# Performance work log

Hardware: AMD Instinct MI355X
Metric: run time of the kernel (lower is better)

## Reference

```python
import jax, jax.numpy as jnp
import numpy as np

D_MODEL = 1024
NUM_HEADS = 16
HEAD_DIM = D_MODEL // NUM_HEADS
B, N = 4, 2048


def setup_inputs() -> dict:
    key = jax.random.key(0)
    ks = jax.random.split(key, 9)
    s = 1.0 / np.sqrt(D_MODEL)
    inp = {
        "x": jax.random.normal(ks[0], (B, N, D_MODEL), dtype=jnp.float32),
        "Wq": jax.random.normal(ks[1], (D_MODEL, D_MODEL), dtype=jnp.float32) * s,
        "bq": jnp.zeros((D_MODEL,), dtype=jnp.float32),
        "Wk": jax.random.normal(ks[2], (D_MODEL, D_MODEL), dtype=jnp.float32) * s,
        "bk": jnp.zeros((D_MODEL,), dtype=jnp.float32),
        "Wv": jax.random.normal(ks[3], (D_MODEL, D_MODEL), dtype=jnp.float32) * s,
        "bv": jnp.zeros((D_MODEL,), dtype=jnp.float32),
        "Wo": jax.random.normal(ks[4], (D_MODEL, D_MODEL), dtype=jnp.float32) * s,
        "bo": jnp.zeros((D_MODEL,), dtype=jnp.float32),
    }
    return inp


def reference(x, Wq, bq, Wk, bk, Wv, bv, Wo, bo):
    b, n, c = x.shape
    h, d = NUM_HEADS, HEAD_DIM
    # QKV projections -> [B, H, N, d]
    q = (x @ Wq + bq).reshape(b, n, h, d).transpose(0, 2, 1, 3)
    k = (x @ Wk + bk).reshape(b, n, h, d).transpose(0, 2, 1, 3)
    v = (x @ Wv + bv).reshape(b, n, h, d).transpose(0, 2, 1, 3)
    scores = jnp.einsum("bhqd,bhkd->bhqk", q, k) / np.sqrt(d).astype(jnp.float32)
    attn = jax.nn.softmax(scores, axis=-1)  # dropout p=0 -> identity
    out = jnp.einsum("bhqk,bhkd->bhqd", attn, v)
    out = out.transpose(0, 2, 1, 3).reshape(b, n, c)
    return out @ Wo + bo
```

## Files before the change

### kernel.cpp

```cpp
#include <hip/hip_runtime.h>
#include <hip/hip_bf16.h>
#include <stdint.h>

#define DM 1024
#define SEQL 2048
#define NBATCH 4
#define NHEAD 16
#define HDIM 64
#define MTOT (NBATCH * SEQL)

using f32x4 = __attribute__((ext_vector_type(4))) float;
using f32x16 = __attribute__((ext_vector_type(16))) float;
using bf16x8 = __attribute__((ext_vector_type(8))) short;

static __device__ __forceinline__ unsigned short f2bf(float f) {
  union { float f; uint32_t u; } v; v.f = f;
  uint32_t u = v.u;
  return (unsigned short)((u + 0x7FFFu + ((u >> 16) & 1u)) >> 16);
}

static __device__ __forceinline__ float exp2_fast(float x) {
#if __has_builtin(__builtin_amdgcn_exp2f)
  return __builtin_amdgcn_exp2f(x);
#else
  float r;
  asm("v_exp_f32 %0, %1" : "=v"(r) : "v"(x));
  return r;
#endif
}

static __device__ __forceinline__ uint32_t pkbf(float lo, float hi) {
  float2 f; f.x = lo; f.y = hi;
  __hip_bfloat162 h = __float22bfloat162_rn(f);
  union { __hip_bfloat162 h; uint32_t u; } cv; cv.h = h;
  return cv.u;
}

static __device__ __forceinline__ f32x16 zero16() {
  f32x16 z;
#pragma unroll
  for (int i = 0; i < 16; ++i) z[i] = 0.f;
  return z;
}

static __device__ __forceinline__ void gload16(const void* g, void* l) {
  __builtin_amdgcn_global_load_lds(
      (const __attribute__((address_space(1))) unsigned int*)g,
      (__attribute__((address_space(3))) unsigned int*)l,
      16, 0, 0);
}

__global__ __launch_bounds__(256) void transpose_convert4(
    const float* __restrict__ W0, const float* __restrict__ W1,
    const float* __restrict__ W2, const float* __restrict__ W3,
    unsigned short* __restrict__ T0, unsigned short* __restrict__ T1,
    unsigned short* __restrict__ T2, unsigned short* __restrict__ T3) {
  __shared__ float tile[64][65];
  const int z = blockIdx.z;
  const float* W = z == 0 ? W0 : z == 1 ? W1 : z == 2 ? W2 : W3;
  unsigned short* WT = z == 0 ? T0 : z == 1 ? T1 : z == 2 ? T2 : T3;
  const int bx = blockIdx.x;
  const int by = blockIdx.y;
  const int t = threadIdx.x;
  const int r = t >> 4;
  const int c4 = (t & 15) * 4;
#pragma unroll
  for (int i = 0; i < 4; ++i) {
    const float4 v = *reinterpret_cast<const float4*>(
        &W[(size_t)(by * 64 + r + i * 16) * DM + bx * 64 + c4]);
    tile[r + i * 16][c4 + 0] = v.x;
    tile[r + i * 16][c4 + 1] = v.y;
    tile[r + i * 16][c4 + 2] = v.z;
    tile[r + i * 16][c4 + 3] = v.w;
  }
  __syncthreads();
#pragma unroll
  for (int i = 0; i < 4; ++i) {
    const int rr = r + i * 16;
    uint32_t lo = (uint32_t)f2bf(tile[c4 + 0][rr]) | ((uint32_t)f2bf(tile[c4 + 1][rr]) << 16);
    uint32_t hi = (uint32_t)f2bf(tile[c4 + 2][rr]) | ((uint32_t)f2bf(tile[c4 + 3][rr]) << 16);
    uint2 o; o.x = lo; o.y = hi;
    *reinterpret_cast<uint2*>(&WT[(size_t)(bx * 64 + rr) * DM + by * 64 + c4]) = o;
  }
}

__global__ __launch_bounds__(256) void convert_x(
    const float* __restrict__ x, unsigned short* __restrict__ xb) {
  const int i = blockIdx.x * 256 + threadIdx.x;
  const float4 v = reinterpret_cast<const float4*>(x)[i];
  uint2 o;
  o.x = (uint32_t)f2bf(v.x) | ((uint32_t)f2bf(v.y) << 16);
  o.y = (uint32_t)f2bf(v.z) | ((uint32_t)f2bf(v.w) << 16);
  reinterpret_cast<uint2*>(xb)[i] = o;
}

#define QSCALE 0.1803368801111204f

__global__ __launch_bounds__(256) void gemm_qkv(
    const unsigned short* __restrict__ A, const unsigned short* __restrict__ BT,
    const float* __restrict__ bq, const float* __restrict__ bk, const float* __restrict__ bv,
    unsigned short* __restrict__ qo, unsigned short* __restrict__ ko,
    unsigned short* __restrict__ vo) {
  __shared__ unsigned short As[128][64];
  __shared__ unsigned short Bs[128][64];
  const int tid = threadIdx.x;
  const int w = tid >> 6;
  const int lane = tid & 63;
  const int wm = w >> 1, wn = w & 1;
  const int m0 = blockIdx.y * 128;
  const int n0 = blockIdx.x * 128;
  const int mode = n0 >> 10;
  const int lrow = lane & 15;
  const int lk = (lane >> 4) * 8;
  const int sRow = lane >> 3;
  const int sCol = (lane & 7) * 8;

  unsigned short* dstA = (mode == 2) ? &Bs[0][0] : &As[0][0];
  unsigned short* dstB = (mode == 2) ? &As[0][0] : &Bs[0][0];

  f32x4 acc[4][4];
#pragma unroll
  for (int m = 0; m < 4; ++m)
#pragma unroll
    for (int n = 0; n < 4; ++n) acc[m][n] = (f32x4){0.f, 0.f, 0.f, 0.f};

  for (int k0 = 0; k0 < DM; k0 += 64) {
#pragma unroll
    for (int i = 0; i < 4; ++i) {
      const int rb = i * 32 + w * 8;
      gload16(&A[(size_t)(m0 + rb + sRow) * DM + k0 + sCol], dstA + rb * 64);
    }
#pragma unroll
    for (int i = 0; i < 4; ++i) {
      const int rb = i * 32 + w * 8;
      gload16(&BT[(size_t)(n0 + rb + sRow) * DM + k0 + sCol], dstB + rb * 64);
    }
    __syncthreads();
#pragma unroll
    for (int ks = 0; ks < 2; ++ks) {
      bf16x8 af[4], bfr[4];
#pragma unroll
      for (int m = 0; m < 4; ++m)
        af[m] = *reinterpret_cast<const bf16x8*>(&As[wm * 64 + m * 16 + lrow][ks * 32 + lk]);
#pragma unroll
      for (int n = 0; n < 4; ++n)
        bfr[n] = *reinterpret_cast<const bf16x8*>(&Bs[wn * 64 + n * 16 + lrow][ks * 32 + lk]);
#pragma unroll
      for (int m = 0; m < 4; ++m)
#pragma unroll
        for (int n = 0; n < 4; ++n)
          acc[m][n] = __builtin_amdgcn_mfma_f32_16x16x32_bf16(af[m], bfr[n], acc[m][n], 0, 0, 0);
    }
    __syncthreads();
  }

  if (mode < 2) {
    const bool isK = (mode == 1);
    unsigned short* dst = isK ? ko : qo;
    const float* bp = isK ? bk : bq;
    const float sc = isK ? 1.f : QSCALE;
#pragma unroll
    for (int n = 0; n < 4; ++n) {
      const int col = (n0 & 1023) + wn * 64 + n * 16 + lrow;
      const float bb = bp[col];
      const int hh = col >> 6, dd = col & 63;
#pragma unroll
      for (int m = 0; m < 4; ++m) {
        const int rowb = m0 + wm * 64 + m * 16 + (lane >> 4) * 4;
#pragma unroll
        for (int r = 0; r < 4; ++r) {
          const int mg = rowb + r;
          const int bidx = mg >> 11;
          const int nn = mg & 2047;
          dst[((size_t)(bidx * NHEAD + hh) * SEQL + nn) * HDIM + dd] =
              f2bf((acc[m][n][r] + bb) * sc);
        }
      }
    }
  } else {
#pragma unroll
    for (int m = 0; m < 4; ++m) {
#pragma unroll
      for (int r = 0; r < 4; ++r) {
        const int dv = (n0 - 2048) + wm * 64 + m * 16 + (lane >> 4) * 4 + r;
        const float bb = bv[dv];
        const int hh = dv >> 6, dd = dv & 63;
#pragma unroll
        for (int n = 0; n < 4; ++n) {
          const int seq = m0 + wn * 64 + n * 16 + lrow;
          const int bidx = seq >> 11;
          const int nn = seq & 2047;
          vo[((size_t)(bidx * NHEAD + hh) * HDIM + dd) * SEQL + nn] =
              f2bf(acc[m][n][r] + bb);
        }
      }
    }
  }
}

__global__ __launch_bounds__(256) void gemm_out(
    const unsigned short* __restrict__ A, const unsigned short* __restrict__ BT,
    const float* __restrict__ bias, float* __restrict__ Cout) {
  __shared__ unsigned short As[128][64];
  __shared__ unsigned short Bs[128][64];
  const int tid = threadIdx.x;
  const int w = tid >> 6;
  const int lane = tid & 63;
  const int wm = w >> 1, wn = w & 1;
  const int m0 = (blockIdx.x >> 3) * 128;
  const int n0 = (blockIdx.x & 7) * 128;
  const int lrow = lane & 15;
  const int lk = (lane >> 4) * 8;
  const int sRow = lane >> 3;
  const int sCol = (lane & 7) * 8;

  f32x4 acc[4][4];
#pragma unroll
  for (int m = 0; m < 4; ++m)
#pragma unroll
    for (int n = 0; n < 4; ++n) acc[m][n] = (f32x4){0.f, 0.f, 0.f, 0.f};

  for (int k0 = 0; k0 < DM; k0 += 64) {
#pragma unroll
    for (int i = 0; i < 4; ++i) {
      const int rb = i * 32 + w * 8;
      gload16(&A[(size_t)(m0 + rb + sRow) * DM + k0 + sCol], &As[rb][0]);
    }
#pragma unroll
    for (int i = 0; i < 4; ++i) {
      const int rb = i * 32 + w * 8;
      gload16(&BT[(size_t)(n0 + rb + sRow) * DM + k0 + sCol], &Bs[rb][0]);
    }
    __syncthreads();
#pragma unroll
    for (int ks = 0; ks < 2; ++ks) {
      bf16x8 af[4], bfr[4];
#pragma unroll
      for (int m = 0; m < 4; ++m)
        af[m] = *reinterpret_cast<const bf16x8*>(&As[wm * 64 + m * 16 + lrow][ks * 32 + lk]);
#pragma unroll
      for (int n = 0; n < 4; ++n)
        bfr[n] = *reinterpret_cast<const bf16x8*>(&Bs[wn * 64 + n * 16 + lrow][ks * 32 + lk]);
#pragma unroll
      for (int m = 0; m < 4; ++m)
#pragma unroll
        for (int n = 0; n < 4; ++n)
          acc[m][n] = __builtin_amdgcn_mfma_f32_16x16x32_bf16(af[m], bfr[n], acc[m][n], 0, 0, 0);
    }
    __syncthreads();
  }

#pragma unroll
  for (int n = 0; n < 4; ++n) {
    const int col = n0 + wn * 64 + n * 16 + lrow;
    const float bb = bias[col];
#pragma unroll
    for (int m = 0; m < 4; ++m) {
      const int rowb = m0 + wm * 64 + m * 16 + (lane >> 4) * 4;
#pragma unroll
      for (int r = 0; r < 4; ++r) {
        Cout[(size_t)(rowb + r) * DM + col] = acc[m][n][r] + bb;
      }
    }
  }
}

__global__ __launch_bounds__(512) void attn_kernel(
    const unsigned short* __restrict__ q, const unsigned short* __restrict__ k,
    const unsigned short* __restrict__ vt, unsigned short* __restrict__ attn_out) {
  __shared__ unsigned short Ks[4][64 * 64];
  __shared__ unsigned short Vs[4][64 * 64];

  const int bid = blockIdx.x;
  const int l0 = (bid & 7) * 64 + (bid >> 3);
  const int bh = l0 >> 3;
  const int qt = l0 & 7;
  const int b = bh >> 4, h = bh & 15;

  const int tid = threadIdx.x;
  const int w = tid >> 6;
  const int lane = tid & 63;
  const int qv = lane & 31;
  const int hi = lane >> 5;
  const int qg0 = qt * 256 + w * 32;

  const unsigned short* qptr = q + (size_t)bh * SEQL * HDIM;
  const unsigned short* kptr = k + (size_t)bh * SEQL * HDIM;
  const unsigned short* vptr = vt + (size_t)bh * HDIM * SEQL;

  bf16x8 qb[4];
#pragma unroll
  for (int kc = 0; kc < 4; ++kc)
    qb[kc] = *reinterpret_cast<const bf16x8*>(&qptr[(qg0 + qv) * HDIM + kc * 16 + hi * 8]);

  bf16x8 ones;
#pragma unroll
  for (int i = 0; i < 8; ++i) ones[i] = (short)0x3F80;

  f32x16 acc0 = zero16(), acc1 = zero16(), accL = zero16();

  const int x7 = qv & 7;
  int off[4];
#pragma unroll
  for (int i = 0; i < 4; ++i) off[i] = ((2 * i + hi) ^ x7) << 3;

  const int srow = tid >> 3;
  const int sslot = tid & 7;
  const int sdst = srow * 64 + ((sslot ^ (srow & 7)) << 3);

  uint4 rk0, rk1, rv0, rv1;
#define LOADT2(rr)                                                                       \
  {                                                                                      \
    rk0 = *reinterpret_cast<const uint4*>(&kptr[((rr) * 128 + srow) * HDIM + sslot * 8]);     \
    rk1 = *reinterpret_cast<const uint4*>(&kptr[((rr) * 128 + 64 + srow) * HDIM + sslot * 8]);\
    rv0 = *reinterpret_cast<const uint4*>(&vptr[srow * SEQL + (rr) * 128 + sslot * 8]);       \
    rv1 = *reinterpret_cast<const uint4*>(&vptr[srow * SEQL + (rr) * 128 + 64 + sslot * 8]);  \
  }

  LOADT2(0);
  const int NR = SEQL / 128;
  for (int r = 0; r < NR; ++r) {
    const int s = (r & 1) << 1;
    *reinterpret_cast<uint4*>(&Ks[s][sdst]) = rk0;
    *reinterpret_cast<uint4*>(&Ks[s + 1][sdst]) = rk1;
    *reinterpret_cast<uint4*>(&Vs[s][sdst]) = rv0;
    *reinterpret_cast<uint4*>(&Vs[s + 1][sdst]) = rv1;
    __syncthreads();
    if (r + 1 < NR) LOADT2(r + 1);

#pragma unroll
    for (int half = 0; half < 2; ++half) {
      const int c = s + half;

      f32x16 p0 = zero16(), p1 = zero16();
      __builtin_amdgcn_s_setprio(1);
#pragma unroll
      for (int kc = 0; kc < 4; ++kc) {
        bf16x8 ka0 = *reinterpret_cast<const bf16x8*>(&Ks[c][qv * 64 + off[kc]]);
        bf16x8 ka1 = *reinterpret_cast<const bf16x8*>(&Ks[c][(32 + qv) * 64 + off[kc]]);
        p0 = __builtin_amdgcn_mfma_f32_32x32x16_bf16(ka0, qb[kc], p0, 0, 0, 0);
        p1 = __builtin_amdgcn_mfma_f32_32x32x16_bf16(ka1, qb[kc], p1, 0, 0, 0);
      }
      __builtin_amdgcn_s_setprio(0);

#pragma unroll
      for (int i = 0; i < 16; ++i) {
        p0[i] = exp2_fast(p0[i]);
        p1[i] = exp2_fast(p1[i]);
      }

      bf16x8 pa[4];
#pragma unroll
      for (int ks = 0; ks < 4; ++ks) {
        const int o = 8 * (ks & 1);
        uint32_t X1, X2, Y1, Y2;
        if (ks < 2) {
          X1 = pkbf(p0[o + 0], p0[o + 1]); X2 = pkbf(p0[o + 2], p0[o + 3]);
          Y1 = pkbf(p0[o + 4], p0[o + 5]); Y2 = pkbf(p0[o + 6], p0[o + 7]);
        } else {
          X1 = pkbf(p1[o + 0], p1[o + 1]); X2 = pkbf(p1[o + 2], p1[o + 3]);
          Y1 = pkbf(p1[o + 4], p1[o + 5]); Y2 = pkbf(p1[o + 6], p1[o + 7]);
        }
        asm("v_permlane32_swap_b32 %0, %1" : "+v"(X1), "+v"(Y1));
        asm("v_permlane32_swap_b32 %0, %1" : "+v"(X2), "+v"(Y2));
        union { uint32_t u[4]; bf16x8 v; } uu;
        uu.u[0] = X1; uu.u[1] = X2; uu.u[2] = Y1; uu.u[3] = Y2;
        pa[ks] = uu.v;
      }

      __builtin_amdgcn_s_setprio(1);
#pragma unroll
      for (int ks = 0; ks < 4; ++ks) {
        bf16x8 vb0 = *reinterpret_cast<const bf16x8*>(&Vs[c][qv * 64 + off[ks]]);
        bf16x8 vb1 = *reinterpret_cast<const bf16x8*>(&Vs[c][(32 + qv) * 64 + off[ks]]);
        acc0 = __builtin_amdgcn_mfma_f32_32x32x16_bf16(pa[ks], vb0, acc0, 0, 0, 0);
        acc1 = __builtin_amdgcn_mfma_f32_32x32x16_bf16(pa[ks], vb1, acc1, 0, 0, 0);
        accL = __builtin_amdgcn_mfma_f32_32x32x16_bf16(pa[ks], ones, accL, 0, 0, 0);
      }
      __builtin_amdgcn_s_setprio(0);
    }
  }
#undef LOADT2

#pragma unroll
  for (int rg = 0; rg < 16; ++rg) {
    const int crow = (rg & 3) + 8 * (rg >> 2) + 4 * hi;
    const float invl = 1.f / accL[rg];
    const int qg = qg0 + crow;
    const size_t base = ((size_t)(b * SEQL + qg) * NHEAD + h) * HDIM + qv;
    attn_out[base] = f2bf(acc0[rg] * invl);
    attn_out[base + 32] = f2bf(acc1[rg] * invl);
  }
}

extern "C" void kernel_launch(void* const* d_in, const int* in_sizes, int n_in,
                              void* d_out, int out_size, void* d_ws, size_t ws_size,
                              hipStream_t stream) {
  const float* x  = (const float*)d_in[0];
  const float* Wq = (const float*)d_in[1];
  const float* bq = (const float*)d_in[2];
  const float* Wk = (const float*)d_in[3];
  const float* bk = (const float*)d_in[4];
  const float* Wv = (const float*)d_in[5];
  const float* bv = (const float*)d_in[6];
  const float* Wo = (const float*)d_in[7];
  const float* bo = (const float*)d_in[8];

  char* ws = (char*)d_ws;
  unsigned short* wqT = (unsigned short*)(ws);
  unsigned short* wkT = wqT + 1024 * 1024;
  unsigned short* wvT = wkT + 1024 * 1024;
  unsigned short* woT = wvT + 1024 * 1024;
  unsigned short* xb   = (unsigned short*)(ws + (size_t)(8 << 20));
  unsigned short* attn = xb;
  unsigned short* qw   = (unsigned short*)(ws + (size_t)(24 << 20));
  unsigned short* kw   = (unsigned short*)(ws + (size_t)(40 << 20));
  unsigned short* vtw  = (unsigned short*)(ws + (size_t)(56 << 20));

  transpose_convert4<<<dim3(16, 16, 4), 256, 0, stream>>>(Wq, Wk, Wv, Wo, wqT, wkT, wvT, woT);
  convert_x<<<MTOT * DM / 4 / 256, 256, 0, stream>>>(x, xb);

  gemm_qkv<<<dim3(24, 64), 256, 0, stream>>>(xb, wqT, bq, bk, bv, qw, kw, vtw);

  attn_kernel<<<512, 512, 0, stream>>>(qw, kw, vtw, attn);

  gemm_out<<<512, 256, 0, stream>>>(attn, woT, bo, (float*)d_out);
}
```

Measured before the change: 202.9 us.

## Double-buffer A tile with XOR swizzle and read weight fragments directly from global

```diff
diff --git a/kernel.cpp b/kernel.cpp
--- a/kernel.cpp
+++ b/kernel.cpp
@@ -101,8 +101,7 @@
     const float* __restrict__ bq, const float* __restrict__ bk, const float* __restrict__ bv,
     unsigned short* __restrict__ qo, unsigned short* __restrict__ ko,
     unsigned short* __restrict__ vo) {
-  __shared__ unsigned short As[128][64];
-  __shared__ unsigned short Bs[128][64];
+  __shared__ unsigned short As[2][128 * 64];
   const int tid = threadIdx.x;
   const int w = tid >> 6;
   const int lane = tid & 63;
@@ -111,12 +110,18 @@
   const int n0 = blockIdx.x * 128;
   const int mode = n0 >> 10;
   const int lrow = lane & 15;
-  const int lk = (lane >> 4) * 8;
+  const int lhi = lane >> 4;
   const int sRow = lane >> 3;
-  const int sCol = (lane & 7) * 8;
-
-  unsigned short* dstA = (mode == 2) ? &Bs[0][0] : &As[0][0];
-  unsigned short* dstB = (mode == 2) ? &As[0][0] : &Bs[0][0];
+  const int sColSwz = (((lane & 7) ^ ((lane >> 3) & 7))) * 8;
+
+#define STAGE_A(tt, bb)                                                        \
+  {                                                                            \
+    const int kk = (tt) * 64;                                                  \
+    _Pragma("unroll") for (int i = 0; i < 4; ++i) {                            \
+      const int rb = i * 32 + w * 8;                                           \
+      gload16(&A[(size_t)(m0 + rb + sRow) * DM + kk + sColSwz], &As[bb][rb * 64]); \
+    }                                                                          \
+  }
 
   f32x4 acc[4][4];
 #pragma unroll
@@ -124,35 +129,47 @@
 #pragma unroll
     for (int n = 0; n < 4; ++n) acc[m][n] = (f32x4){0.f, 0.f, 0.f, 0.f};
 
-  for (int k0 = 0; k0 < DM; k0 += 64) {
-#pragma unroll
-    for (int i = 0; i < 4; ++i) {
-      const int rb = i * 32 + w * 8;
-      gload16(&A[(size_t)(m0 + rb + sRow) * DM + k0 + sCol], dstA + rb * 64);
-    }
-#pragma unroll
-    for (int i = 0; i < 4; ++i) {
-      const int rb = i * 32 + w * 8;
-      gload16(&BT[(size_t)(n0 + rb + sRow) * DM + k0 + sCol], dstB + rb * 64);
-    }
-    __syncthreads();
+  STAGE_A(0, 0);
+  __syncthreads();
+
+  const int NK = DM / 64;
+  for (int t = 0; t < NK; ++t) {
+    const int bu = t & 1;
+    if (t + 1 < NK) STAGE_A(t + 1, bu ^ 1);
+    const int k0 = t * 64;
 #pragma unroll
     for (int ks = 0; ks < 2; ++ks) {
       bf16x8 af[4], bfr[4];
 #pragma unroll
-      for (int m = 0; m < 4; ++m)
-        af[m] = *reinterpret_cast<const bf16x8*>(&As[wm * 64 + m * 16 + lrow][ks * 32 + lk]);
+      for (int m = 0; m < 4; ++m) {
+        const int r = wm * 64 + m * 16 + lrow;
+        af[m] = *reinterpret_cast<const bf16x8*>(
+            &As[bu][r * 64 + (((ks * 4 + lhi) ^ (lrow & 7)) << 3)]);
+      }
 #pragma unroll
       for (int n = 0; n < 4; ++n)
-        bfr[n] = *reinterpret_cast<const bf16x8*>(&Bs[wn * 64 + n * 16 + lrow][ks * 32 + lk]);
-#pragma unroll
-      for (int m = 0; m < 4; ++m)
+        bfr[n] = *reinterpret_cast<const bf16x8*>(
+            &BT[(size_t)(n0 + wn * 64 + n * 16 + lrow) * DM + k0 + ks * 32 + lhi * 8]);
+
+      __builtin_amdgcn_s_setprio(1);
+      if (mode == 2) {
 #pragma unroll
         for (int n = 0; n < 4; ++n)
-          acc[m][n] = __builtin_amdgcn_mfma_f32_16x16x32_bf16(af[m], bfr[n], acc[m][n], 0, 0, 0);
+#pragma unroll
+          for (int m = 0; m < 4; ++m)
+            acc[n][m] = __builtin_amdgcn_mfma_f32_16x16x32_bf16(bfr[n], af[m], acc[n][m], 0, 0, 0);
+      } else {
+#pragma unroll
+        for (int m = 0; m < 4; ++m)
+#pragma unroll
+          for (int n = 0; n < 4; ++n)
+            acc[m][n] = __builtin_amdgcn_mfma_f32_16x16x32_bf16(af[m], bfr[n], acc[m][n], 0, 0, 0);
+      }
+      __builtin_amdgcn_s_setprio(0);
     }
     __syncthreads();
   }
+#undef STAGE_A
 
   if (mode < 2) {
     const bool isK = (mode == 1);
@@ -166,7 +183,7 @@
       const int hh = col >> 6, dd = col & 63;
 #pragma unroll
       for (int m = 0; m < 4; ++m) {
-        const int rowb = m0 + wm * 64 + m * 16 + (lane >> 4) * 4;
+        const int rowb = m0 + wm * 64 + m * 16 + lhi * 4;
 #pragma unroll
         for (int r = 0; r < 4; ++r) {
           const int mg = rowb + r;
@@ -179,19 +196,19 @@
     }
   } else {
 #pragma unroll
-    for (int m = 0; m < 4; ++m) {
+    for (int n = 0; n < 4; ++n) {
 #pragma unroll
       for (int r = 0; r < 4; ++r) {
-        const int dv = (n0 - 2048) + wm * 64 + m * 16 + (lane >> 4) * 4 + r;
+        const int dv = (n0 - 2048) + wn * 64 + n * 16 + lhi * 4 + r;
         const float bb = bv[dv];
         const int hh = dv >> 6, dd = dv & 63;
 #pragma unroll
-        for (int n = 0; n < 4; ++n) {
-          const int seq = m0 + wn * 64 + n * 16 + lrow;
+        for (int m = 0; m < 4; ++m) {
+          const int seq = m0 + wm * 64 + m * 16 + lrow;
           const int bidx = seq >> 11;
           const int nn = seq & 2047;
           vo[((size_t)(bidx * NHEAD + hh) * HDIM + dd) * SEQL + nn] =
-              f2bf(acc[m][n][r] + bb);
+              f2bf(acc[n][m][r] + bb);
         }
       }
     }
```

New measurement: 231.5 us. 14.1% more time.
